# Optimization experiments

Measured on AMD Instinct MI355X. Metric: run time of the kernel, lower is better.

Reference implementation:

```python
import jax, jax.numpy as jnp
import numpy as np


def _xavier(key, shape):
    fan_out, fan_in = shape
    lim = float(np.sqrt(6.0 / (fan_in + fan_out)))
    return jax.random.uniform(key, shape, jnp.float32, -lim, lim)


def setup_inputs() -> dict:
    B, I, H, P = 8192, 1024, 1024, 2048
    key = jax.random.key(0)
    ks = jax.random.split(key, 12)
    return {
        "x": jax.random.normal(ks[0], (B, I), jnp.float32),
        "hidden": jax.random.normal(ks[1], (B, H), jnp.float32),
        "persistent_memory": jax.random.normal(ks[2], (B, P), jnp.float32),
        # attention_gate: Linear(H,H), 'gate' bias init = -0.1
        "Wa": _xavier(ks[3], (H, H)), "ba": jnp.full((H,), -0.1, jnp.float32),
        # reset/update/new gates: Linear(I+H, H), 'gate' bias init = -0.1
        "Wr": _xavier(ks[4], (H, I + H)), "br": jnp.full((H,), -0.1, jnp.float32),
        "Wu": _xavier(ks[5], (H, I + H)), "bu": jnp.full((H,), -0.1, jnp.float32),
        "Wn": _xavier(ks[6], (H, I + H)), "bn": jnp.full((H,), -0.1, jnp.float32),
        # memory read/write/address: Linear(H,P), zero bias; forget bias = 1.0
        "Wread": _xavier(ks[7], (P, H)), "bread": jnp.zeros((P,), jnp.float32),
        "Wwrite": _xavier(ks[8], (P, H)), "bwrite": jnp.zeros((P,), jnp.float32),
        "Wforget": _xavier(ks[9], (P, H)), "bforget": jnp.ones((P,), jnp.float32),
        "Waddr": _xavier(ks[10], (P, H)), "baddr": jnp.zeros((P,), jnp.float32),
        "connection_strength": jnp.ones((H,), jnp.float32),
        "connection_decay": jnp.full((1,), 0.99, jnp.float32),
        "connection_history": jnp.zeros((H,), jnp.float32),  # buffer, starts at 0
    }


def reference(x, hidden, persistent_memory, Wa, ba, Wr, br, Wu, bu, Wn, bn,
              Wread, bread, Wwrite, bwrite, Wforget, bforget, Waddr, baddr,
              connection_strength, connection_decay, connection_history):
    H = hidden.shape[1]
    # update_connections (reward=None): history*decay + detached mean(|h|) over batch
    activity = jax.lax.stop_gradient(jnp.mean(jnp.abs(hidden), axis=0))  # [H]
    ch = connection_history * connection_decay + activity
    cs = connection_strength * jax.nn.sigmoid(ch)  # [H]

    attention = jax.nn.sigmoid(hidden @ Wa.T + ba)
    ha = hidden * attention
    combined = jnp.concatenate([x, ha], axis=1)
    reset = combined @ Wr.T + br
    update = combined @ Wu.T + bu
    combined_reset = jnp.concatenate([x, reset * ha], axis=1)
    new = combined_reset @ Wn.T + bn
    # neuromodulators=None: apply_neuromodulation returns gates UNACTIVATED (faithful)
    hidden_new = (1.0 - update) * hidden + update * new * cs[None, :]  # [B,H]

    addr = jax.nn.softmax(hidden_new @ Waddr.T + baddr, axis=1)        # [B,P]
    read = jax.nn.sigmoid(hidden_new @ Wread.T + bread)
    write = jax.nn.sigmoid(hidden_new @ Wwrite.T + bwrite)
    forget = jax.nn.sigmoid(hidden_new @ Wforget.T + bforget)

    # F.linear with ones(P,H)/H weight == row-mean of hidden_new broadcast to P
    hp = jnp.mean(hidden_new, axis=1, keepdims=True)                   # [B,1]
    memory_new = forget * persistent_memory + write * hp * addr        # [B,P]
    memory_read_content = read * memory_new
    # F.linear with ones(H,P)/P weight == row-mean over P broadcast to H
    hidden_final = hidden_new + jnp.mean(memory_read_content, axis=1, keepdims=True)
    return hidden_final, memory_new
```

## Files before the change

kernel.cpp:

```cpp
#include <hip/hip_runtime.h>

typedef unsigned short u16;
typedef short bfrag __attribute__((ext_vector_type(8)));
typedef float f32x4 __attribute__((ext_vector_type(4)));
typedef const __attribute__((address_space(1))) unsigned int* gp1_t;
typedef __attribute__((address_space(3))) unsigned int* lp3_t;

#define B_ 8192
#define H_ 1024
#define P_ 2048

__device__ __forceinline__ u16 f2bf(float f) {
  unsigned u = __builtin_bit_cast(unsigned, f);
  u += 0x7fffu + ((u >> 16) & 1u);
  return (u16)(u >> 16);
}
__device__ __forceinline__ float bf2f(u16 s) {
  return __builtin_bit_cast(float, (unsigned)s << 16);
}
__device__ __forceinline__ float sigm(float v) { return 1.f / (1.f + __expf(-v)); }


__global__ void k_hidact(const float* __restrict__ hidden, u16* __restrict__ hB,
                         float* __restrict__ act) {
  const int t = threadIdx.x;
  const int r0 = blockIdx.x * 16;
  float s00 = 0, s01 = 0, s10 = 0, s11 = 0;
  for (int r = 0; r < 16; ++r) {
    const float* q = hidden + (size_t)(r0 + r) * H_;
    u16* o = hB + (size_t)(r0 + r) * H_;
    float2 v0 = *(const float2*)&q[2 * t];
    float2 v1 = *(const float2*)&q[512 + 2 * t];
    s00 += fabsf(v0.x); s01 += fabsf(v0.y);
    s10 += fabsf(v1.x); s11 += fabsf(v1.y);
    ushort2 o0, o1;
    o0.x = f2bf(v0.x); o0.y = f2bf(v0.y);
    o1.x = f2bf(v1.x); o1.y = f2bf(v1.y);
    *(ushort2*)&o[2 * t] = o0;
    *(ushort2*)&o[512 + 2 * t] = o1;
  }
  atomicAdd(&act[2 * t], s00); atomicAdd(&act[2 * t + 1], s01);
  atomicAdd(&act[512 + 2 * t], s10); atomicAdd(&act[512 + 2 * t + 1], s11);
}

__global__ void k_cs(const float* __restrict__ act, const float* __restrict__ strength,
                     const float* __restrict__ decay, const float* __restrict__ hist,
                     float* __restrict__ cs) {
  int h = blockIdx.x * 256 + threadIdx.x;
  float ch = hist[h] * decay[0] + act[h] * (1.f / (float)B_);
  cs[h] = strength[h] * sigm(ch);
}

struct ConvPs {
  const float* s[9];
  u16* d[9];
  int n4[9];
};

__global__ void k_conv9(ConvPs p) {
  const int e = blockIdx.y;
  const int n4 = p.n4[e];
  const float4* s = (const float4*)p.s[e];
  ushort4* d = (ushort4*)p.d[e];
  for (int i = blockIdx.x * 256 + threadIdx.x; i < n4; i += 2048 * 256) {
    float4 v = s[i];
    ushort4 o;
    o.x = f2bf(v.x); o.y = f2bf(v.y); o.z = f2bf(v.z); o.w = f2bf(v.w);
    d[i] = o;
  }
}

__global__ void k_rowmean(const float* __restrict__ hn, float* __restrict__ hp) {
  int row = blockIdx.x * 4 + (threadIdx.x >> 6);
  int lane = threadIdx.x & 63;
  const float* p = hn + (size_t)row * H_;
  float s = 0.f;
#pragma unroll
  for (int c = 0; c < H_ / 64; ++c) s += p[lane + c * 64];
#pragma unroll
  for (int o = 32; o; o >>= 1) s += __shfl_down(s, o);
  if (lane == 0) hp[row] = s * (1.f / (float)H_);
}


struct GemmPs {
  const u16* Bm[4];
  const float* bias[4];
  const float* hidden;
  const float* update;
  const float* cs;
  const u16* haB;
  u16* rhaB;
  float* out_f1;
  float* hn_f32;
  u16* hn_bf16;
  u16* haB_out;
  u16* out_b[4];
};

template <int EPI>
__device__ __forceinline__ void epi(int row, int col, float v, int z, const GemmPs& e) {
  if constexpr (EPI == 1) {
    v += e.bias[0][col];
    float a = sigm(v);
    size_t i = (size_t)row * H_ + col;
    e.haB_out[i] = f2bf(e.hidden[i] * a);
  } else if constexpr (EPI == 2) {
    size_t i = (size_t)row * H_ + col;
    if (z == 0) {
      v += e.bias[0][col];
      e.rhaB[i] = f2bf(v * bf2f(e.haB[i]));
    } else {
      v += e.bias[1][col];
      e.out_f1[i] = v;
    }
  } else if constexpr (EPI == 3) {
    v += e.bias[0][col];
    size_t i = (size_t)row * H_ + col;
    float u = e.update[i];
    float hn = (1.f - u) * e.hidden[i] + u * v * e.cs[col];
    e.hn_f32[i] = hn;
    e.hn_bf16[i] = f2bf(hn);
  } else {
    v += e.bias[z][col];
    e.out_b[z][(size_t)row * P_ + col] = f2bf(v);
  }
}


template <int EPI>
__global__ __launch_bounds__(256, 2) void gemm_bt(const u16* __restrict__ A0,
                                                  const u16* __restrict__ A1,
                                                  int K0, int K, GemmPs e) {
  const int z = blockIdx.z;
  const u16* __restrict__ Bm = e.Bm[z];
  __shared__ u16 As[128 * 64];
  __shared__ u16 Bs[128 * 64];
  const int lane = threadIdx.x & 63;
  const int w = threadIdx.x >> 6;
  const int wr = w >> 1, wc = w & 1;
  const int m0 = blockIdx.x * 128, n0 = blockIdx.y * 128;

  f32x4 acc[4][4] = {};

  const int rA = lane >> 3;
  const int srcSlot8 = ((lane & 7) ^ (rA & 7)) << 3;

  const int g = lane >> 4;
  const int r15 = lane & 15;
  const int rx = lane & 7;

  for (int k0 = 0; k0 < K; k0 += 64) {
    const u16* Ab; int sA, kl;
    if (k0 < K0) { Ab = A0; sA = K0; kl = k0; }
    else         { Ab = A1; sA = K - K0; kl = k0 - K0; }
    const u16* pA = Ab + (size_t)(m0 + w * 32 + rA) * sA + kl + srcSlot8;
    const u16* pB = Bm + (size_t)(n0 + w * 32 + rA) * K + k0 + srcSlot8;
#pragma unroll
    for (int j = 0; j < 4; ++j) {
      __builtin_amdgcn_global_load_lds((gp1_t)(pA + (size_t)j * 8 * sA),
                                       (lp3_t)&As[(w * 32 + j * 8) * 64], 16, 0, 0);
      __builtin_amdgcn_global_load_lds((gp1_t)(pB + (size_t)j * 8 * K),
                                       (lp3_t)&Bs[(w * 32 + j * 8) * 64], 16, 0, 0);
    }
    asm volatile("s_waitcnt vmcnt(0)" ::: "memory");
    __syncthreads();
#pragma unroll
    for (int kk = 0; kk < 64; kk += 32) {
      const int slot = g + (kk >> 3);
      const int cswz = ((slot ^ rx) << 3);
      bfrag af[4], bq[4];
#pragma unroll
      for (int i = 0; i < 4; ++i) {
        af[i] = *(const bfrag*)&As[(wr * 64 + i * 16 + r15) * 64 + cswz];
        bq[i] = *(const bfrag*)&Bs[(wc * 64 + i * 16 + r15) * 64 + cswz];
      }
#pragma unroll
      for (int mi = 0; mi < 4; ++mi)
#pragma unroll
        for (int ni = 0; ni < 4; ++ni)
          acc[mi][ni] = __builtin_amdgcn_mfma_f32_16x16x32_bf16(af[mi], bq[ni], acc[mi][ni], 0, 0, 0);
    }
    __syncthreads();
  }

#pragma unroll
  for (int mi = 0; mi < 4; ++mi)
#pragma unroll
    for (int ni = 0; ni < 4; ++ni)
#pragma unroll
      for (int r = 0; r < 4; ++r)
        epi<EPI>(m0 + wr * 64 + mi * 16 + g * 4 + r,
                 n0 + wc * 64 + ni * 16 + r15, acc[mi][ni][r], z, e);
}


#define QUAD(Af, Bf, MO, NO)                                                         \
  do {                                                                               \
    _Pragma("unroll") for (int ks = 0; ks < 2; ++ks)                                 \
    _Pragma("unroll") for (int mi = 0; mi < 4; ++mi)                                 \
    _Pragma("unroll") for (int ni = 0; ni < 2; ++ni)                                 \
      acc[(MO) + mi][(NO) + ni] = __builtin_amdgcn_mfma_f32_16x16x32_bf16(           \
          Af[mi][ks], Bf[ni][ks], acc[(MO) + mi][(NO) + ni], 0, 0, 0);               \
  } while (0)

#define LGKM0()                                           \
  do {                                                    \
    asm volatile("s_waitcnt lgkmcnt(0)" ::: "memory");    \
    __builtin_amdgcn_sched_barrier(0);                    \
  } while (0)

template <int EPI>
__global__ __launch_bounds__(512, 2) void gemm8(const u16* __restrict__ A0,
                                                const u16* __restrict__ A1,
                                                int K0, int K, GemmPs e) {
  __shared__ u16 As[2][256 * 64];
  __shared__ u16 Bs[2][256 * 64];
  const int z = blockIdx.z;
  const u16* __restrict__ Bw = e.Bm[z];

  const int bid = blockIdx.x;
  const int xcd = bid & 7, jj = bid >> 3;
  const int m0 = (xcd * 4 + (jj & 3)) << 8;
  const int n0 = (jj >> 2) << 8;

  const int tid = threadIdx.x;
  const int lane = tid & 63;
  const int w = tid >> 6;
  const int wr = w >> 2, wc = w & 3;
  const int r15 = lane & 15, g = lane >> 4, rx = lane & 7;

  const int srow = tid >> 3;
  const int sslot8 = ((tid & 7) ^ (srow & 7)) << 3;

  f32x4 acc[8][4] = {};

  auto stageA = [&](int buf, int kt) {
    const int k0 = kt << 6;
    const u16* Ab; int sA, kl;
    if (k0 < K0) { Ab = A0; sA = K0; kl = k0; }
    else         { Ab = A1; sA = K - K0; kl = k0 - K0; }
    const u16* pa = Ab + (size_t)(m0 + srow) * sA + kl + sslot8;
    u16* la = &As[buf][(w * 8) * 64];
#pragma unroll
    for (int r = 0; r < 4; ++r)
      __builtin_amdgcn_global_load_lds((gp1_t)(pa + (size_t)(r * 64) * sA),
                                       (lp3_t)(la + r * 64 * 64), 16, 0, 0);
  };
  auto stageB = [&](int buf, int kt) {
    const int k0 = kt << 6;
    const u16* pb = Bw + (size_t)(n0 + srow) * K + k0 + sslot8;
    u16* lb = &Bs[buf][(w * 8) * 64];
#pragma unroll
    for (int r = 0; r < 4; ++r)
      __builtin_amdgcn_global_load_lds((gp1_t)(pb + (size_t)(r * 64) * K),
                                       (lp3_t)(lb + r * 64 * 64), 16, 0, 0);
  };

  const int nt = K >> 6;
  stageA(0, 0); stageB(0, 0);
  stageA(1, 1); stageB(1, 1);
  asm volatile("s_waitcnt vmcnt(8)" ::: "memory");
  __builtin_amdgcn_s_barrier();

  bfrag af[4][2], b0[2][2], b1[2][2];

  for (int t = 0; t < nt; ++t) {
    const int buf = t & 1;
#pragma unroll
    for (int mi = 0; mi < 4; ++mi)
#pragma unroll
      for (int ks = 0; ks < 2; ++ks)
        af[mi][ks] = *(const bfrag*)&As[buf][(wr * 128 + mi * 16 + r15) * 64 +
                                            (((g + ks * 4) ^ rx) << 3)];
#pragma unroll
    for (int ni = 0; ni < 2; ++ni)
#pragma unroll
      for (int ks = 0; ks < 2; ++ks)
        b0[ni][ks] = *(const bfrag*)&Bs[buf][(wc * 64 + ni * 16 + r15) * 64 +
                                            (((g + ks * 4) ^ rx) << 3)];
    __builtin_amdgcn_s_barrier();
    LGKM0();
    __builtin_amdgcn_s_setprio(1);
    QUAD(af, b0, 0, 0);
    __builtin_amdgcn_s_setprio(0);
    __builtin_amdgcn_s_barrier();
#pragma unroll
    for (int ni = 0; ni < 2; ++ni)
#pragma unroll
      for (int ks = 0; ks < 2; ++ks)
        b1[ni][ks] = *(const bfrag*)&Bs[buf][(wc * 64 + 32 + ni * 16 + r15) * 64 +
                                            (((g + ks * 4) ^ rx) << 3)];
    __builtin_amdgcn_s_barrier();
    LGKM0();
    __builtin_amdgcn_s_setprio(1);
    QUAD(af, b1, 0, 2);
    __builtin_amdgcn_s_setprio(0);
    __builtin_amdgcn_s_barrier();
    if (t + 2 < nt) stageB(buf, t + 2);
#pragma unroll
    for (int mi = 0; mi < 4; ++mi)
#pragma unroll
      for (int ks = 0; ks < 2; ++ks)
        af[mi][ks] = *(const bfrag*)&As[buf][(wr * 128 + 64 + mi * 16 + r15) * 64 +
                                            (((g + ks * 4) ^ rx) << 3)];
    __builtin_amdgcn_s_barrier();
    LGKM0();
    __builtin_amdgcn_s_setprio(1);
    QUAD(af, b0, 4, 0);
    __builtin_amdgcn_s_setprio(0);
    __builtin_amdgcn_s_barrier();
    if (t + 2 < nt) {
      stageA(buf, t + 2);
      asm volatile("s_waitcnt vmcnt(8)" ::: "memory");
    } else {
      asm volatile("s_waitcnt vmcnt(0)" ::: "memory");
    }
    __builtin_amdgcn_s_barrier();
    __builtin_amdgcn_s_setprio(1);
    QUAD(af, b1, 4, 2);
    __builtin_amdgcn_s_setprio(0);
    __builtin_amdgcn_s_barrier();
  }

#pragma unroll
  for (int mi = 0; mi < 8; ++mi)
#pragma unroll
    for (int ni = 0; ni < 4; ++ni)
#pragma unroll
      for (int rr = 0; rr < 4; ++rr)
        epi<EPI>(m0 + wr * 128 + mi * 16 + g * 4 + rr,
                 n0 + wc * 64 + ni * 16 + r15, acc[mi][ni][rr], z, e);
}


__global__ __launch_bounds__(256) void k_final(
    const u16* __restrict__ aL, const u16* __restrict__ rL,
    const u16* __restrict__ wL, const u16* __restrict__ fL,
    const float* __restrict__ pm, const float* __restrict__ hn,
    const float* __restrict__ hp, float* __restrict__ outH, float* __restrict__ outM) {
  __shared__ float sl[P_];
  __shared__ float red[8];
  const int row = blockIdx.x, t = threadIdx.x;
  const size_t base = (size_t)row * P_;

  float lm = -3.4e38f;
  for (int p = t; p < P_; p += 256) {
    float v = bf2f(aL[base + p]);
    sl[p] = v;
    lm = fmaxf(lm, v);
  }
#pragma unroll
  for (int o = 32; o; o >>= 1) lm = fmaxf(lm, __shfl_down(lm, o));
  if ((t & 63) == 0) red[t >> 6] = lm;
  __syncthreads();
  const float bmax = fmaxf(fmaxf(red[0], red[1]), fmaxf(red[2], red[3]));

  float ls = 0.f;
  for (int p = t; p < P_; p += 256) {
    float ev = __expf(sl[p] - bmax);
    sl[p] = ev;
    ls += ev;
  }
#pragma unroll
  for (int o = 32; o; o >>= 1) ls += __shfl_down(ls, o);
  if ((t & 63) == 0) red[4 + (t >> 6)] = ls;
  __syncthreads();
  const float inv = 1.f / (red[4] + red[5] + red[6] + red[7]);
  const float hpv = hp[row];

  float rs = 0.f;
  for (int p = t; p < P_; p += 256) {
    float a = sl[p] * inv;
    float fo = sigm(bf2f(fL[base + p]));
    float wv = sigm(bf2f(wL[base + p]));
    float rd = sigm(bf2f(rL[base + p]));
    float mem = fo * pm[base + p] + wv * hpv * a;
    outM[base + p] = mem;
    rs += rd * mem;
  }
#pragma unroll
  for (int o = 32; o; o >>= 1) rs += __shfl_down(rs, o);
  __syncthreads();
  if ((t & 63) == 0) red[t >> 6] = rs;
  __syncthreads();
  const float mean = (red[0] + red[1] + red[2] + red[3]) * (1.f / (float)P_);
  const size_t hb = (size_t)row * H_;
  for (int h = t; h < H_; h += 256) outH[hb + h] = hn[hb + h] + mean;
}


extern "C" void kernel_launch(void* const* d_in, const int* in_sizes, int n_in,
                              void* d_out, int out_size, void* d_ws, size_t ws_size,
                              hipStream_t stream) {
  (void)in_sizes; (void)n_in; (void)out_size; (void)ws_size;
  const float* x       = (const float*)d_in[0];
  const float* hidden  = (const float*)d_in[1];
  const float* pm      = (const float*)d_in[2];
  const float* Wa      = (const float*)d_in[3];
  const float* ba      = (const float*)d_in[4];
  const float* Wr      = (const float*)d_in[5];
  const float* br      = (const float*)d_in[6];
  const float* Wu      = (const float*)d_in[7];
  const float* bu      = (const float*)d_in[8];
  const float* Wn      = (const float*)d_in[9];
  const float* bn      = (const float*)d_in[10];
  const float* Wread   = (const float*)d_in[11];
  const float* bread   = (const float*)d_in[12];
  const float* Wwrite  = (const float*)d_in[13];
  const float* bwrite  = (const float*)d_in[14];
  const float* Wforget = (const float*)d_in[15];
  const float* bforget = (const float*)d_in[16];
  const float* Waddr   = (const float*)d_in[17];
  const float* baddr   = (const float*)d_in[18];
  const float* cstr    = (const float*)d_in[19];
  const float* cdecay  = (const float*)d_in[20];
  const float* chist   = (const float*)d_in[21];

  char* wsp = (char*)d_ws;
  auto take = [&](size_t n) { char* p = wsp; wsp += (n + 255) & ~(size_t)255; return p; };
  float* act    = (float*)take((size_t)H_ * 4);
  float* cs     = (float*)take((size_t)H_ * 4);
  float* hp     = (float*)take((size_t)B_ * 4);
  u16* hiddenB  = (u16*)take((size_t)B_ * H_ * 2);
  u16* xB       = (u16*)take((size_t)B_ * H_ * 2);
  u16* haB      = (u16*)take((size_t)B_ * H_ * 2);
  u16* rhaB     = (u16*)take((size_t)B_ * H_ * 2);
  u16* WaB      = (u16*)take((size_t)H_ * H_ * 2);
  u16* WrB      = (u16*)take((size_t)H_ * 2048 * 2);
  u16* WuB      = (u16*)take((size_t)H_ * 2048 * 2);
  u16* WnB      = (u16*)take((size_t)H_ * 2048 * 2);
  u16* WadB     = (u16*)take((size_t)P_ * H_ * 2);
  u16* WrdB     = (u16*)take((size_t)P_ * H_ * 2);
  u16* WwrB     = (u16*)take((size_t)P_ * H_ * 2);
  u16* WfgB     = (u16*)take((size_t)P_ * H_ * 2);
  float* update = (float*)take((size_t)B_ * H_ * 4);
  float* hnf    = (float*)take((size_t)B_ * H_ * 4);
  u16* gAd      = (u16*)take((size_t)B_ * P_ * 2);
  u16* gRd      = (u16*)take((size_t)B_ * P_ * 2);
  u16* gWr      = (u16*)take((size_t)B_ * P_ * 2);
  u16* gFg      = (u16*)take((size_t)B_ * P_ * 2);

  float* outH = (float*)d_out;
  float* outM = outH + (size_t)B_ * H_;

  hipMemsetAsync(act, 0, (size_t)H_ * 4, stream);
  k_hidact<<<dim3(512), dim3(256), 0, stream>>>(hidden, hiddenB, act);
  k_cs<<<dim3(4), dim3(256), 0, stream>>>(act, cstr, cdecay, chist, cs);

  {
    ConvPs p;
    const float* ss[9] = {Wa, Wr, Wu, Wn, Waddr, Wread, Wwrite, Wforget, x};
    u16* dd[9] = {WaB, WrB, WuB, WnB, WadB, WrdB, WwrB, WfgB, xB};
    int nn[9] = {H_ * H_ / 4, H_ * 2048 / 4, H_ * 2048 / 4, H_ * 2048 / 4,
                 P_ * H_ / 4, P_ * H_ / 4, P_ * H_ / 4, P_ * H_ / 4, B_ * H_ / 4};
    for (int i = 0; i < 9; ++i) { p.s[i] = ss[i]; p.d[i] = dd[i]; p.n4[i] = nn[i]; }
    k_conv9<<<dim3(2048, 9), dim3(256), 0, stream>>>(p);
  }

  {
    GemmPs e{};
    e.Bm[0] = WaB; e.bias[0] = ba; e.hidden = hidden; e.haB_out = haB;
    gemm_bt<1><<<dim3(64, 8, 1), dim3(256), 0, stream>>>(hiddenB, hiddenB, 1024, 1024, e);
  }
  {
    GemmPs e{};
    e.Bm[0] = WrB; e.Bm[1] = WuB; e.bias[0] = br; e.bias[1] = bu;
    e.haB = haB; e.rhaB = rhaB; e.out_f1 = update;
    gemm_bt<2><<<dim3(64, 8, 2), dim3(256), 0, stream>>>(xB, haB, 1024, 2048, e);
  }
  {
    GemmPs e{};
    e.Bm[0] = WnB; e.bias[0] = bn; e.hidden = hidden; e.update = update; e.cs = cs;
    e.hn_f32 = hnf; e.hn_bf16 = hiddenB;
    gemm_bt<3><<<dim3(64, 8, 1), dim3(256), 0, stream>>>(xB, rhaB, 1024, 2048, e);
  }
  k_rowmean<<<dim3(2048), dim3(256), 0, stream>>>(hnf, hp);
  {
    GemmPs e{};
    e.Bm[0] = WadB; e.Bm[1] = WrdB; e.Bm[2] = WwrB; e.Bm[3] = WfgB;
    e.bias[0] = baddr; e.bias[1] = bread; e.bias[2] = bwrite; e.bias[3] = bforget;
    e.out_b[0] = gAd; e.out_b[1] = gRd; e.out_b[2] = gWr; e.out_b[3] = gFg;
    gemm8<4><<<dim3(256, 1, 4), dim3(512), 0, stream>>>(hiddenB, hiddenB, 1024, 1024, e);
  }
  k_final<<<dim3(B_), dim3(256), 0, stream>>>(gAd, gRd, gWr, gFg, pm, hnf, hp, outH, outM);
}
```

Measured before the change: 451.0 us.

## Transpose MFMA operands for vectorized epilogues and interleave staged loads

Swaps the MFMA A/B operands so each lane holds four consecutive output columns. The GEMM epilogues can then do float4/ushort4 loads and stores instead of scattered scalar accesses. The gemm8 prefetch is split into per-row loads spread across the compute phases to smooth memory issue. k_final and k_rowmean are rewritten to keep one row in registers with vectorized loads, which drops the LDS buffer; this relies on fixed P=2048 and 256 threads.

```diff
diff --git a/kernel.cpp b/kernel.cpp
--- a/kernel.cpp
+++ b/kernel.cpp
@@ -73,10 +73,13 @@
 __global__ void k_rowmean(const float* __restrict__ hn, float* __restrict__ hp) {
   int row = blockIdx.x * 4 + (threadIdx.x >> 6);
   int lane = threadIdx.x & 63;
-  const float* p = hn + (size_t)row * H_;
+  const float4* p4 = (const float4*)(hn + (size_t)row * H_);
   float s = 0.f;
 #pragma unroll
-  for (int c = 0; c < H_ / 64; ++c) s += p[lane + c * 64];
+  for (int c = 0; c < 4; ++c) {
+    float4 v = p4[lane + c * 64];
+    s += v.x + v.y + v.z + v.w;
+  }
 #pragma unroll
   for (int o = 32; o; o >>= 1) s += __shfl_down(s, o);
   if (lane == 0) hp[row] = s * (1.f / (float)H_);
@@ -99,31 +102,55 @@
 };
 
 template <int EPI>
-__device__ __forceinline__ void epi(int row, int col, float v, int z, const GemmPs& e) {
+__device__ __forceinline__ void epiV(int row, int col0, f32x4 v, int z, const GemmPs& e) {
   if constexpr (EPI == 1) {
-    v += e.bias[0][col];
-    float a = sigm(v);
-    size_t i = (size_t)row * H_ + col;
-    e.haB_out[i] = f2bf(e.hidden[i] * a);
+    float4 bi = *(const float4*)&e.bias[0][col0];
+    size_t i = (size_t)row * H_ + col0;
+    float4 hd = *(const float4*)&e.hidden[i];
+    ushort4 o;
+    o.x = f2bf(hd.x * sigm(v[0] + bi.x));
+    o.y = f2bf(hd.y * sigm(v[1] + bi.y));
+    o.z = f2bf(hd.z * sigm(v[2] + bi.z));
+    o.w = f2bf(hd.w * sigm(v[3] + bi.w));
+    *(ushort4*)&e.haB_out[i] = o;
   } else if constexpr (EPI == 2) {
-    size_t i = (size_t)row * H_ + col;
+    size_t i = (size_t)row * H_ + col0;
     if (z == 0) {
-      v += e.bias[0][col];
-      e.rhaB[i] = f2bf(v * bf2f(e.haB[i]));
+      float4 bi = *(const float4*)&e.bias[0][col0];
+      ushort4 h = *(const ushort4*)&e.haB[i];
+      ushort4 o;
+      o.x = f2bf((v[0] + bi.x) * bf2f(h.x));
+      o.y = f2bf((v[1] + bi.y) * bf2f(h.y));
+      o.z = f2bf((v[2] + bi.z) * bf2f(h.z));
+      o.w = f2bf((v[3] + bi.w) * bf2f(h.w));
+      *(ushort4*)&e.rhaB[i] = o;
     } else {
-      v += e.bias[1][col];
-      e.out_f1[i] = v;
+      float4 bi = *(const float4*)&e.bias[1][col0];
+      float4 o;
+      o.x = v[0] + bi.x; o.y = v[1] + bi.y; o.z = v[2] + bi.z; o.w = v[3] + bi.w;
+      *(float4*)&e.out_f1[i] = o;
     }
   } else if constexpr (EPI == 3) {
-    v += e.bias[0][col];
-    size_t i = (size_t)row * H_ + col;
-    float u = e.update[i];
-    float hn = (1.f - u) * e.hidden[i] + u * v * e.cs[col];
-    e.hn_f32[i] = hn;
-    e.hn_bf16[i] = f2bf(hn);
+    float4 bi = *(const float4*)&e.bias[0][col0];
+    size_t i = (size_t)row * H_ + col0;
+    float4 u4 = *(const float4*)&e.update[i];
+    float4 hd = *(const float4*)&e.hidden[i];
+    float4 c4 = *(const float4*)&e.cs[col0];
+    float4 hn;
+    hn.x = (1.f - u4.x) * hd.x + u4.x * (v[0] + bi.x) * c4.x;
+    hn.y = (1.f - u4.y) * hd.y + u4.y * (v[1] + bi.y) * c4.y;
+    hn.z = (1.f - u4.z) * hd.z + u4.z * (v[2] + bi.z) * c4.z;
+    hn.w = (1.f - u4.w) * hd.w + u4.w * (v[3] + bi.w) * c4.w;
+    *(float4*)&e.hn_f32[i] = hn;
+    ushort4 o;
+    o.x = f2bf(hn.x); o.y = f2bf(hn.y); o.z = f2bf(hn.z); o.w = f2bf(hn.w);
+    *(ushort4*)&e.hn_bf16[i] = o;
   } else {
-    v += e.bias[z][col];
-    e.out_b[z][(size_t)row * P_ + col] = f2bf(v);
+    float4 bi = *(const float4*)&e.bias[z][col0];
+    ushort4 o;
+    o.x = f2bf(v[0] + bi.x); o.y = f2bf(v[1] + bi.y);
+    o.z = f2bf(v[2] + bi.z); o.w = f2bf(v[3] + bi.w);
+    *(ushort4*)&e.out_b[z][(size_t)row * P_ + col0] = o;
   }
 }
 
@@ -179,7 +206,7 @@
       for (int mi = 0; mi < 4; ++mi)
 #pragma unroll
         for (int ni = 0; ni < 4; ++ni)
-          acc[mi][ni] = __builtin_amdgcn_mfma_f32_16x16x32_bf16(af[mi], bq[ni], acc[mi][ni], 0, 0, 0);
+          acc[mi][ni] = __builtin_amdgcn_mfma_f32_16x16x32_bf16(bq[ni], af[mi], acc[mi][ni], 0, 0, 0);
     }
     __syncthreads();
   }
@@ -188,10 +215,8 @@
   for (int mi = 0; mi < 4; ++mi)
 #pragma unroll
     for (int ni = 0; ni < 4; ++ni)
-#pragma unroll
-      for (int r = 0; r < 4; ++r)
-        epi<EPI>(m0 + wr * 64 + mi * 16 + g * 4 + r,
-                 n0 + wc * 64 + ni * 16 + r15, acc[mi][ni][r], z, e);
+      epiV<EPI>(m0 + wr * 64 + mi * 16 + r15,
+                n0 + wc * 64 + ni * 16 + g * 4, acc[mi][ni], z, e);
 }
 
 
@@ -201,7 +226,7 @@
     _Pragma("unroll") for (int mi = 0; mi < 4; ++mi)                                 \
     _Pragma("unroll") for (int ni = 0; ni < 2; ++ni)                                 \
       acc[(MO) + mi][(NO) + ni] = __builtin_amdgcn_mfma_f32_16x16x32_bf16(           \
-          Af[mi][ks], Bf[ni][ks], acc[(MO) + mi][(NO) + ni], 0, 0, 0);               \
+          Bf[ni][ks], Af[mi][ks], acc[(MO) + mi][(NO) + ni], 0, 0, 0);               \
   } while (0)
 
 #define LGKM0()                                           \
@@ -235,31 +260,27 @@
 
   f32x4 acc[8][4] = {};
 
-  auto stageA = [&](int buf, int kt) {
+  auto stageA1 = [&](int buf, int kt, int r) {
     const int k0 = kt << 6;
     const u16* Ab; int sA, kl;
     if (k0 < K0) { Ab = A0; sA = K0; kl = k0; }
     else         { Ab = A1; sA = K - K0; kl = k0 - K0; }
-    const u16* pa = Ab + (size_t)(m0 + srow) * sA + kl + sslot8;
-    u16* la = &As[buf][(w * 8) * 64];
-#pragma unroll
-    for (int r = 0; r < 4; ++r)
-      __builtin_amdgcn_global_load_lds((gp1_t)(pa + (size_t)(r * 64) * sA),
-                                       (lp3_t)(la + r * 64 * 64), 16, 0, 0);
+    const u16* pa = Ab + (size_t)(m0 + srow + r * 64) * sA + kl + sslot8;
+    __builtin_amdgcn_global_load_lds((gp1_t)pa,
+                                     (lp3_t)&As[buf][(w * 8 + r * 64) * 64], 16, 0, 0);
   };
-  auto stageB = [&](int buf, int kt) {
+  auto stageB1 = [&](int buf, int kt, int r) {
     const int k0 = kt << 6;
-    const u16* pb = Bw + (size_t)(n0 + srow) * K + k0 + sslot8;
-    u16* lb = &Bs[buf][(w * 8) * 64];
-#pragma unroll
-    for (int r = 0; r < 4; ++r)
-      __builtin_amdgcn_global_load_lds((gp1_t)(pb + (size_t)(r * 64) * K),
-                                       (lp3_t)(lb + r * 64 * 64), 16, 0, 0);
+    const u16* pb = Bw + (size_t)(n0 + srow + r * 64) * K + k0 + sslot8;
+    __builtin_amdgcn_global_load_lds((gp1_t)pb,
+                                     (lp3_t)&Bs[buf][(w * 8 + r * 64) * 64], 16, 0, 0);
   };
 
   const int nt = K >> 6;
-  stageA(0, 0); stageB(0, 0);
-  stageA(1, 1); stageB(1, 1);
+#pragma unroll
+  for (int r = 0; r < 4; ++r) { stageA1(0, 0, r); stageB1(0, 0, r); }
+#pragma unroll
+  for (int r = 0; r < 4; ++r) { stageA1(1, 1, r); stageB1(1, 1, r); }
   asm volatile("s_waitcnt vmcnt(8)" ::: "memory");
   __builtin_amdgcn_s_barrier();
 
@@ -267,6 +288,7 @@
 
   for (int t = 0; t < nt; ++t) {
     const int buf = t & 1;
+    const bool pf = (t + 2 < nt);
 #pragma unroll
     for (int mi = 0; mi < 4; ++mi)
 #pragma unroll
@@ -291,27 +313,31 @@
       for (int ks = 0; ks < 2; ++ks)
         b1[ni][ks] = *(const bfrag*)&Bs[buf][(wc * 64 + 32 + ni * 16 + r15) * 64 +
                                             (((g + ks * 4) ^ rx) << 3)];
+    if (pf) { stageA1(buf, t + 2, 0); stageA1(buf, t + 2, 2); }
     __builtin_amdgcn_s_barrier();
     LGKM0();
     __builtin_amdgcn_s_setprio(1);
     QUAD(af, b1, 0, 2);
     __builtin_amdgcn_s_setprio(0);
     __builtin_amdgcn_s_barrier();
-    if (t + 2 < nt) stageB(buf, t + 2);
 #pragma unroll
     for (int mi = 0; mi < 4; ++mi)
 #pragma unroll
       for (int ks = 0; ks < 2; ++ks)
         af[mi][ks] = *(const bfrag*)&As[buf][(wr * 128 + 64 + mi * 16 + r15) * 64 +
                                             (((g + ks * 4) ^ rx) << 3)];
+    if (pf) {
+      stageB1(buf, t + 2, 0); stageB1(buf, t + 2, 1);
+      stageB1(buf, t + 2, 2); stageB1(buf, t + 2, 3);
+    }
     __builtin_amdgcn_s_barrier();
     LGKM0();
     __builtin_amdgcn_s_setprio(1);
     QUAD(af, b0, 4, 0);
     __builtin_amdgcn_s_setprio(0);
     __builtin_amdgcn_s_barrier();
-    if (t + 2 < nt) {
-      stageA(buf, t + 2);
+    if (pf) {
+      stageA1(buf, t + 2, 1); stageA1(buf, t + 2, 3);
       asm volatile("s_waitcnt vmcnt(8)" ::: "memory");
     } else {
       asm volatile("s_waitcnt vmcnt(0)" ::: "memory");
@@ -327,10 +353,8 @@
   for (int mi = 0; mi < 8; ++mi)
 #pragma unroll
     for (int ni = 0; ni < 4; ++ni)
-#pragma unroll
-      for (int rr = 0; rr < 4; ++rr)
-        epi<EPI>(m0 + wr * 128 + mi * 16 + g * 4 + rr,
-                 n0 + wc * 64 + ni * 16 + r15, acc[mi][ni][rr], z, e);
+      epiV<EPI>(m0 + wr * 128 + mi * 16 + r15,
+                n0 + wc * 64 + ni * 16 + g * 4, acc[mi][ni], z, e);
 }
 
 
@@ -339,54 +363,66 @@
     const u16* __restrict__ wL, const u16* __restrict__ fL,
     const float* __restrict__ pm, const float* __restrict__ hn,
     const float* __restrict__ hp, float* __restrict__ outH, float* __restrict__ outM) {
-  __shared__ float sl[P_];
   __shared__ float red[8];
   const int row = blockIdx.x, t = threadIdx.x;
-  const size_t base = (size_t)row * P_;
-
-  float lm = -3.4e38f;
-  for (int p = t; p < P_; p += 256) {
-    float v = bf2f(aL[base + p]);
-    sl[p] = v;
-    lm = fmaxf(lm, v);
-  }
-#pragma unroll
-  for (int o = 32; o; o >>= 1) lm = fmaxf(lm, __shfl_down(lm, o));
+  const size_t base = (size_t)row * P_ + t * 8;
+
+  ushort4 a0 = *(const ushort4*)&aL[base];
+  ushort4 a1 = *(const ushort4*)&aL[base + 4];
+  float av[8] = {bf2f(a0.x), bf2f(a0.y), bf2f(a0.z), bf2f(a0.w),
+                 bf2f(a1.x), bf2f(a1.y), bf2f(a1.z), bf2f(a1.w)};
+  float lm = av[0];
+#pragma unroll
+  for (int j = 1; j < 8; ++j) lm = fmaxf(lm, av[j]);
+#pragma unroll
+  for (int o = 32; o; o >>= 1) lm = fmaxf(lm, __shfl_xor(lm, o));
   if ((t & 63) == 0) red[t >> 6] = lm;
   __syncthreads();
   const float bmax = fmaxf(fmaxf(red[0], red[1]), fmaxf(red[2], red[3]));
 
+  float ev[8];
   float ls = 0.f;
-  for (int p = t; p < P_; p += 256) {
-    float ev = __expf(sl[p] - bmax);
-    sl[p] = ev;
-    ls += ev;
-  }
-#pragma unroll
-  for (int o = 32; o; o >>= 1) ls += __shfl_down(ls, o);
+#pragma unroll
+  for (int j = 0; j < 8; ++j) { ev[j] = __expf(av[j] - bmax); ls += ev[j]; }
+#pragma unroll
+  for (int o = 32; o; o >>= 1) ls += __shfl_xor(ls, o);
   if ((t & 63) == 0) red[4 + (t >> 6)] = ls;
   __syncthreads();
   const float inv = 1.f / (red[4] + red[5] + red[6] + red[7]);
   const float hpv = hp[row];
 
+  ushort4 r0 = *(const ushort4*)&rL[base], r1 = *(const ushort4*)&rL[base + 4];
+  ushort4 w0 = *(const ushort4*)&wL[base], w1 = *(const ushort4*)&wL[base + 4];
+  ushort4 f0 = *(const ushort4*)&fL[base], f1 = *(const ushort4*)&fL[base + 4];
+  float4 p0 = *(const float4*)&pm[base], p1 = *(const float4*)&pm[base + 4];
+  float rv[8] = {bf2f(r0.x), bf2f(r0.y), bf2f(r0.z), bf2f(r0.w),
+                 bf2f(r1.x), bf2f(r1.y), bf2f(r1.z), bf2f(r1.w)};
+  float wv[8] = {bf2f(w0.x), bf2f(w0.y), bf2f(w0.z), bf2f(w0.w),
+                 bf2f(w1.x), bf2f(w1.y), bf2f(w1.z), bf2f(w1.w)};
+  float fv[8] = {bf2f(f0.x), bf2f(f0.y), bf2f(f0.z), bf2f(f0.w),
+                 bf2f(f1.x), bf2f(f1.y), bf2f(f1.z), bf2f(f1.w)};
+  float pv[8] = {p0.x, p0.y, p0.z, p0.w, p1.x, p1.y, p1.z, p1.w};
+  float mem[8];
   float rs = 0.f;
-  for (int p = t; p < P_; p += 256) {
-    float a = sl[p] * inv;
-    float fo = sigm(bf2f(fL[base + p]));
-    float wv = sigm(bf2f(wL[base + p]));
-    float rd = sigm(bf2f(rL[base + p]));
-    float mem = fo * pm[base + p] + wv * hpv * a;
-    outM[base + p] = mem;
-    rs += rd * mem;
-  }
-#pragma unroll
-  for (int o = 32; o; o >>= 1) rs += __shfl_down(rs, o);
+#pragma unroll
+  for (int j = 0; j < 8; ++j) {
+    mem[j] = sigm(fv[j]) * pv[j] + sigm(wv[j]) * hpv * (ev[j] * inv);
+    rs += sigm(rv[j]) * mem[j];
+  }
+  float4 m0v = {mem[0], mem[1], mem[2], mem[3]};
+  float4 m1v = {mem[4], mem[5], mem[6], mem[7]};
+  *(float4*)&outM[base] = m0v;
+  *(float4*)&outM[base + 4] = m1v;
+#pragma unroll
+  for (int o = 32; o; o >>= 1) rs += __shfl_xor(rs, o);
   __syncthreads();
   if ((t & 63) == 0) red[t >> 6] = rs;
   __syncthreads();
   const float mean = (red[0] + red[1] + red[2] + red[3]) * (1.f / (float)P_);
-  const size_t hb = (size_t)row * H_;
-  for (int h = t; h < H_; h += 256) outH[hb + h] = hn[hb + h] + mean;
+  const size_t hb = (size_t)row * H_ + t * 4;
+  float4 h4 = *(const float4*)&hn[hb];
+  h4.x += mean; h4.y += mean; h4.z += mean; h4.w += mean;
+  *(float4*)&outH[hb] = h4;
 }
 
 
```

Result: no change. 449.0 us (-0.4%).
